# Performance work log

Hardware: AMD Instinct MI355X
Metric: run time of the kernel (lower is better)

## Reference

```python
import jax, jax.numpy as jnp
import numpy as np

SIZE = (4096, 4096)   # self.size
SIGMA = 1.0           # blur_sigma
NOISE_STD = 0.01      # noise_std


def _gauss_kernel(sigma):
    # scipy.ndimage.gaussian_filter: radius = int(truncate*sigma + 0.5), truncate=4.0
    r = int(4.0 * sigma + 0.5)
    x = np.arange(-r, r + 1, dtype=np.float32)
    k = np.exp(-0.5 * (x / sigma) ** 2)
    k = k / k.sum()
    return jnp.asarray(k), r


def _blur(img, sigma):
    # img: [C, H, W]; separable Gaussian, scipy mode='reflect' == jnp symmetric pad
    k, r = _gauss_kernel(sigma)
    x = jnp.pad(img, ((0, 0), (r, r), (r, r)), mode='symmetric')
    x = x[:, None]  # [C, 1, H+2r, W+2r] (NCHW)
    kh = k.reshape(1, 1, -1, 1)
    kw = k.reshape(1, 1, 1, -1)
    x = jax.lax.conv_general_dilated(x, kh, (1, 1), 'VALID')
    x = jax.lax.conv_general_dilated(x, kw, (1, 1), 'VALID')
    return x[:, 0]  # [C, H, W]


def setup_inputs() -> dict:
    key = jax.random.key(0)
    k1, k2 = jax.random.split(key)
    img = jax.random.normal(k1, (1, 2048, 2048), dtype=jnp.float32)
    noise = jax.random.normal(k2, (1,) + SIZE, dtype=jnp.float32)
    return {"img": img, "noise": noise}


def reference(img, noise):
    # bilinear resize, align_corners=False == jax half-pixel linear resize
    img = jax.image.resize(img, (img.shape[0],) + SIZE, method='linear')
    img = jnp.flip(img, axis=2)   # horizontal flip
    img = jnp.flip(img, axis=1)   # vertical flip
    img = jnp.rot90(img, k=1, axes=(1, 2))  # rot90, k fixed to 1
    img = img + noise * NOISE_STD
    img = _blur(img, SIGMA)
    img = jnp.log1p(jnp.clip(img, 0.0))  # clamp(min=0) then log1p
    return img
```

## Files before the change

kernel.cpp:

```cpp
#include <hip/hip_runtime.h>
#include <math.h>

#define N      4096
#define NIMG   2048
#define SPAN   128
#define TXN    120
#define HRW    16
#define PP     66
#define PR     68
#define IPOFF  (PR * PP)
#define NSX    35
#define NSY    64
#define NBLK   (NSX * NSY)

#define KW0 0.00013383063f
#define KW1 0.00443186160f
#define KW2 0.05399112800f
#define KW3 0.24197144000f
#define KW4 0.39894346870f

__device__ __forceinline__ int symi(int g) {
    g = (g < 0) ? (-1 - g) : g;
    g = (g >= N) ? (2 * N - 1 - g) : g;
    return g;
}

__device__ __forceinline__ void gload_lds4(const float* g, float* l) {
    __builtin_amdgcn_global_load_lds(
        (const __attribute__((address_space(1))) unsigned int*)g,
        (__attribute__((address_space(3))) unsigned int*)l, 4, 0, 0);
}

#define H9(A,B,C,D,E,F,G,H,I)                                                  \
    fmaf(KW0,(A), fmaf(KW1,(B), fmaf(KW2,(C), fmaf(KW3,(D), fmaf(KW4,(E),      \
    fmaf(KW3,(F), fmaf(KW2,(G), fmaf(KW1,(H), KW0*(I)))))))))

#define GCOL2(J, G) do {                                                       \
    const float p0_ = ipg[(J) - PP];                                           \
    const float p1_ = ipg[(J)];                                                \
    const float p2_ = ipg[(J) + PP];                                           \
    (G).x = fmaf(0.75f, p1_, 0.25f * p2_);                                     \
    (G).y = fmaf(0.25f, p0_, 0.75f * p1_);                                     \
} while (0)

#define PROD4(J2, D0, D1, D2, D3, Z0, Z1, Z2, Z3) do {                         \
    float2 gc_, gd_;                                                           \
    GCOL2((J2), gc_); GCOL2((J2) + 1, gd_);                                    \
    (D0).x = fmaf(0.25f, ga.x, fmaf(0.75f, gb.x, 0.01f * (Z0).x));             \
    (D0).y = fmaf(0.25f, ga.y, fmaf(0.75f, gb.y, 0.01f * (Z0).y));             \
    (D1).x = fmaf(0.75f, gb.x, fmaf(0.25f, gc_.x, 0.01f * (Z1).x));            \
    (D1).y = fmaf(0.75f, gb.y, fmaf(0.25f, gc_.y, 0.01f * (Z1).y));            \
    (D2).x = fmaf(0.25f, gb.x, fmaf(0.75f, gc_.x, 0.01f * (Z2).x));            \
    (D2).y = fmaf(0.25f, gb.y, fmaf(0.75f, gc_.y, 0.01f * (Z2).y));            \
    (D3).x = fmaf(0.75f, gc_.x, fmaf(0.25f, gd_.x, 0.01f * (Z3).x));           \
    (D3).y = fmaf(0.75f, gc_.y, fmaf(0.25f, gd_.y, 0.01f * (Z3).y));           \
    ga = gc_; gb = gd_;                                                        \
} while (0)

#define OUT1(K, GY) do {                                                       \
    float2 v_;                                                                 \
    v_.x = H9(win[K].x, win[K+1].x, win[K+2].x, win[K+3].x, win[K+4].x,        \
              win[K+5].x, win[K+6].x, win[K+7].x, win[K+8].x);                 \
    v_.y = H9(win[K].y, win[K+1].y, win[K+2].y, win[K+3].y, win[K+4].y,        \
              win[K+5].y, win[K+6].y, win[K+7].y, win[K+8].y);                 \
    float* sl_ = ((K) & 1) ? EX1 : EX0;                                        \
    *reinterpret_cast<float2*>(sl_ + 2 * lane) = v_;                           \
    const float2 l0_ = *reinterpret_cast<const float2*>(sl_ + oL0);            \
    const float2 l1_ = *reinterpret_cast<const float2*>(sl_ + oL1);            \
    const float2 r0_ = *reinterpret_cast<const float2*>(sl_ + oR0);            \
    const float2 r1_ = *reinterpret_cast<const float2*>(sl_ + oR1);            \
    float ox_ = KW0 * l0_.x; ox_ = fmaf(KW1, l0_.y, ox_);                      \
    ox_ = fmaf(KW2, l1_.x, ox_); ox_ = fmaf(KW3, l1_.y, ox_);                  \
    ox_ = fmaf(KW4, v_.x, ox_);  ox_ = fmaf(KW3, v_.y, ox_);                   \
    ox_ = fmaf(KW2, r0_.x, ox_); ox_ = fmaf(KW1, r0_.y, ox_);                  \
    ox_ = fmaf(KW0, r1_.x, ox_);                                               \
    float oy_ = KW0 * l0_.y; oy_ = fmaf(KW1, l1_.x, oy_);                      \
    oy_ = fmaf(KW2, l1_.y, oy_); oy_ = fmaf(KW3, v_.x, oy_);                   \
    oy_ = fmaf(KW4, v_.y, oy_);  oy_ = fmaf(KW3, r0_.x, oy_);                  \
    oy_ = fmaf(KW2, r0_.y, oy_); oy_ = fmaf(KW1, r1_.x, oy_);                  \
    oy_ = fmaf(KW0, r1_.y, oy_);                                               \
    float2 rr_;                                                                \
    rr_.x = __logf(1.0f + fmaxf(ox_, 0.0f));                                   \
    rr_.y = __logf(1.0f + fmaxf(oy_, 0.0f));                                   \
    if (okst) *reinterpret_cast<float2*>(out + (size_t)(GY) * N + gxs) = rr_;  \
} while (0)

#define SLIDE4() do {                                                          \
    _Pragma("unroll")                                                          \
    for (int i_ = 0; i_ < 8; ++i_) win[i_] = win[i_ + 4];                      \
} while (0)

__global__ __launch_bounds__(256, 6)
void TensorAugment_79216376807666_kernel(const float* __restrict__ img,
                                         const float* __restrict__ noise,
                                         float* __restrict__ out) {
    __shared__ __align__(16) float SH[IPOFF + 4 * 256];

    const int tid  = threadIdx.x;
    const int lane = tid & 63;
    const int wave = tid >> 6;

    float* const IP  = SH;
    float* const EX0 = SH + IPOFF + wave * 256;
    float* const EX1 = EX0 + 128;

    const int bid = blockIdx.x;
    int sx, sy;
    if (bid < 2 * NSY) { sy = bid >> 1; sx = (bid & 1) ? (NSX - 1) : 0; }
    else { const int t = bid - 2 * NSY; sx = 1 + t % (NSX - 2); sy = t / (NSX - 2); }
    const int x0 = sx * TXN;
    const int y0 = sy * 64;

    int gxa = x0 - 4, gxb = x0 + SPAN - 5;
    int mxa = symi(gxa), mxb = symi(gxb);
    int gxmin = min(mxa, mxb), gxmax = max(mxa, mxb);
    if (gxa <= 0) gxmin = 0;
    if (gxb >= N - 1) gxmax = N - 1;
    int umin = (N - 1) - gxmax, umax = (N - 1) - gxmin;
    int r0min = (umin - 1) >> 1;
    int r0max = (umax - 1) >> 1;
    int nrows = r0max - r0min + 2;

    int gya = y0 - 4, gyb = y0 + 67;
    int mya = symi(gya), myb = symi(gyb);
    int gymin = min(mya, myb), gymax = max(mya, myb);
    if (gya <= 0) gymin = 0;
    if (gyb >= N - 1) gymax = N - 1;
    int c0min = (gymin - 1) >> 1;
    (void)nrows;

    {
        const int gcol = min(max(c0min + lane, 0), NIMG - 1);
#pragma unroll
        for (int k = 0; k < 17; ++k) {
            const int r  = wave + 4 * k;
            const int ir = min(max(r0min + r, 0), NIMG - 1);
            gload_lds4(img + (size_t)ir * NIMG + gcol, IP + r * PP);
        }
    }

    const int y0w = y0 + HRW * wave;
    const int gxs = x0 - 4 + 2 * lane;
    const bool okst = (lane >= 2) && (lane <= 61) && (gxs <= N - 2);
    const bool yin  = (y0w >= 4) && (y0w + 19 <= N - 1);
    const bool xin  = (sx > 0) && (sx < NSX - 1);
    const bool fast = xin && yin;
    const int oL0 = max(2 * lane - 4, 0), oL1 = max(2 * lane - 2, 0);
    const int oR0 = min(2 * lane + 2, 126), oR1 = min(2 * lane + 4, 126);

    const int a    = (x0 >> 1) - 2 + lane;
    const int ipb  = (2047 - a - r0min) * PP;
    const float* const ipg = IP + ipb;
    const int jb   = ((y0w - 5) >> 1) - c0min;
    const float* const nzb = noise + ((size_t)(y0w - 4) * N + gxs);
#define LDNZ(DR) (*reinterpret_cast<const float2*>(nzb + (size_t)(DR) * N))

    float2 npre[12];
    if (fast) {
#pragma unroll
        for (int j = 0; j < 12; ++j) npre[j] = LDNZ(j);
    }

    __syncthreads();

    float2 win[12];

    if (fast) {
        float2 ga, gb;
        GCOL2(jb, ga);
        GCOL2(jb + 1, gb);

        PROD4(jb + 2, win[0], win[1], win[2],  win[3],  npre[0], npre[1], npre[2],  npre[3]);
        PROD4(jb + 4, win[4], win[5], win[6],  win[7],  npre[4], npre[5], npre[6],  npre[7]);
        PROD4(jb + 6, win[8], win[9], win[10], win[11], npre[8], npre[9], npre[10], npre[11]);

        {
            float2 n0 = LDNZ(12), n1 = LDNZ(13), n2 = LDNZ(14), n3 = LDNZ(15);
            OUT1(0, y0w + 0); OUT1(1, y0w + 1); OUT1(2, y0w + 2); OUT1(3, y0w + 3);
            SLIDE4();
            PROD4(jb + 8, win[8], win[9], win[10], win[11], n0, n1, n2, n3);
        }
        {
            float2 n0 = LDNZ(16), n1 = LDNZ(17), n2 = LDNZ(18), n3 = LDNZ(19);
            OUT1(0, y0w + 4); OUT1(1, y0w + 5); OUT1(2, y0w + 6); OUT1(3, y0w + 7);
            SLIDE4();
            PROD4(jb + 10, win[8], win[9], win[10], win[11], n0, n1, n2, n3);
        }
        {
            float2 n0 = LDNZ(20), n1 = LDNZ(21), n2 = LDNZ(22), n3 = LDNZ(23);
            OUT1(0, y0w + 8); OUT1(1, y0w + 9); OUT1(2, y0w + 10); OUT1(3, y0w + 11);
            SLIDE4();
            PROD4(jb + 12, win[8], win[9], win[10], win[11], n0, n1, n2, n3);
        }
        OUT1(0, y0w + 12); OUT1(1, y0w + 13); OUT1(2, y0w + 14); OUT1(3, y0w + 15);
    } else {
        const int gxm0 = symi(gxs), gxm1 = symi(gxs + 1);
        const int u0 = (N - 1) - gxm0, u1 = (N - 1) - gxm1;
        const int A0 = (((u0 - 1) >> 1) - r0min) * PP;
        const int A1 = (((u1 - 1) >> 1) - r0min) * PP;
        const float w10 = (u0 & 1) ? 0.25f : 0.75f, w00 = 1.0f - w10;
        const float w11 = (u1 & 1) ? 0.25f : 0.75f, w01 = 1.0f - w11;

        auto nzg = [&](int dr) -> float2 {
            const float* nr = noise + (size_t)symi(y0w - 4 + dr) * N;
            float2 r; r.x = nr[gxm0]; r.y = nr[gxm1]; return r;
        };
        auto dgen = [&](int dr, float2 nz) -> float2 {
            const int gym = symi(y0w - 4 + dr);
            const int jc  = ((gym - 1) >> 1) - c0min;
            const float wc1 = (gym & 1) ? 0.25f : 0.75f;
            const float wc0 = 1.0f - wc1;
            float2 r;
            {
                const float t = fmaf(wc0, IP[A0 + jc], wc1 * IP[A0 + jc + 1]);
                const float b = fmaf(wc0, IP[A0 + PP + jc], wc1 * IP[A0 + PP + jc + 1]);
                r.x = fmaf(w00, t, fmaf(w10, b, 0.01f * nz.x));
            }
            {
                const float t = fmaf(wc0, IP[A1 + jc], wc1 * IP[A1 + jc + 1]);
                const float b = fmaf(wc0, IP[A1 + PP + jc], wc1 * IP[A1 + PP + jc + 1]);
                r.y = fmaf(w01, t, fmaf(w11, b, 0.01f * nz.y));
            }
            return r;
        };

#pragma unroll
        for (int j = 0; j < 12; ++j) win[j] = dgen(j, nzg(j));

#pragma unroll
        for (int c = 0; c < 4; ++c) {
            float2 n0, n1, n2, n3;
            if (c < 3) { n0 = nzg(12 + 4 * c); n1 = nzg(13 + 4 * c);
                         n2 = nzg(14 + 4 * c); n3 = nzg(15 + 4 * c); }
            OUT1(0, y0w + 4 * c + 0); OUT1(1, y0w + 4 * c + 1);
            OUT1(2, y0w + 4 * c + 2); OUT1(3, y0w + 4 * c + 3);
            if (c < 3) {
                SLIDE4();
                win[8]  = dgen(12 + 4 * c, n0);
                win[9]  = dgen(13 + 4 * c, n1);
                win[10] = dgen(14 + 4 * c, n2);
                win[11] = dgen(15 + 4 * c, n3);
            }
        }
    }
#undef LDNZ
}

extern "C" void kernel_launch(void* const* d_in, const int* in_sizes, int n_in,
                              void* d_out, int out_size, void* d_ws, size_t ws_size,
                              hipStream_t stream) {
    const float* img   = (const float*)d_in[0];
    const float* noise = (const float*)d_in[1];
    float* out = (float*)d_out;

    dim3 grid(NBLK);
    TensorAugment_79216376807666_kernel<<<grid, 256, 0, stream>>>(img, noise, out);
}
```

Measured before the change: 144.0 us.

## Swap LDS direct loads for register staging, remap blocks per XCD, prefetch noise earlier

```diff
diff --git a/kernel.cpp b/kernel.cpp
--- a/kernel.cpp
+++ b/kernel.cpp
@@ -7,8 +7,7 @@
 #define TXN    120
 #define HRW    16
 #define PP     66
-#define PR     68
-#define IPOFF  (PR * PP)
+#define PR     66
 #define NSX    35
 #define NSY    64
 #define NBLK   (NSX * NSY)
@@ -23,12 +22,6 @@
     g = (g < 0) ? (-1 - g) : g;
     g = (g >= N) ? (2 * N - 1 - g) : g;
     return g;
-}
-
-__device__ __forceinline__ void gload_lds4(const float* g, float* l) {
-    __builtin_amdgcn_global_load_lds(
-        (const __attribute__((address_space(1))) unsigned int*)g,
-        (__attribute__((address_space(3))) unsigned int*)l, 4, 0, 0);
 }
 
 #define H9(A,B,C,D,E,F,G,H,I)                                                  \
@@ -90,26 +83,27 @@
     for (int i_ = 0; i_ < 8; ++i_) win[i_] = win[i_ + 4];                      \
 } while (0)
 
-__global__ __launch_bounds__(256, 6)
+__global__ __launch_bounds__(256, 5)
 void TensorAugment_79216376807666_kernel(const float* __restrict__ img,
                                          const float* __restrict__ noise,
                                          float* __restrict__ out) {
-    __shared__ __align__(16) float SH[IPOFF + 4 * 256];
+    __shared__ __align__(16) float SH[PR * PP + 4 * 256];
 
     const int tid  = threadIdx.x;
     const int lane = tid & 63;
     const int wave = tid >> 6;
 
     float* const IP  = SH;
-    float* const EX0 = SH + IPOFF + wave * 256;
+    float* const EX0 = SH + PR * PP + wave * 256;
     float* const EX1 = EX0 + 128;
 
-    const int bid = blockIdx.x;
-    int sx, sy;
-    if (bid < 2 * NSY) { sy = bid >> 1; sx = (bid & 1) ? (NSX - 1) : 0; }
-    else { const int t = bid - 2 * NSY; sx = 1 + t % (NSX - 2); sy = t / (NSX - 2); }
-    const int x0 = sx * TXN;
-    const int y0 = sy * 64;
+    const int bid0 = blockIdx.x;
+    const int xcd  = bid0 & 7;
+    const int ii   = bid0 >> 3;
+    const int sx   = ii % NSX;
+    const int sy   = xcd * (NSY / 8) + ii / NSX;
+    const int x0   = sx * TXN;
+    const int y0   = sy * 64;
 
     int gxa = x0 - 4, gxb = x0 + SPAN - 5;
     int mxa = symi(gxa), mxb = symi(gxb);
@@ -127,15 +121,20 @@
     if (gya <= 0) gymin = 0;
     if (gyb >= N - 1) gymax = N - 1;
     int c0min = (gymin - 1) >> 1;
-    (void)nrows;
 
     {
         const int gcol = min(max(c0min + lane, 0), NIMG - 1);
+        float sv[17];
 #pragma unroll
         for (int k = 0; k < 17; ++k) {
-            const int r  = wave + 4 * k;
+            const int r  = min(wave + 4 * k, nrows - 1);
             const int ir = min(max(r0min + r, 0), NIMG - 1);
-            gload_lds4(img + (size_t)ir * NIMG + gcol, IP + r * PP);
+            sv[k] = img[(size_t)ir * NIMG + gcol];
+        }
+#pragma unroll
+        for (int k = 0; k < 17; ++k) {
+            const int r = min(wave + 4 * k, nrows - 1);
+            IP[r * PP + lane] = sv[k];
         }
     }
 
@@ -156,9 +155,11 @@
 #define LDNZ(DR) (*reinterpret_cast<const float2*>(nzb + (size_t)(DR) * N))
 
     float2 npre[12];
+    float2 nA0, nA1, nA2, nA3;
     if (fast) {
 #pragma unroll
         for (int j = 0; j < 12; ++j) npre[j] = LDNZ(j);
+        nA0 = LDNZ(12); nA1 = LDNZ(13); nA2 = LDNZ(14); nA3 = LDNZ(15);
     }
 
     __syncthreads();
@@ -166,6 +167,8 @@
     float2 win[12];
 
     if (fast) {
+        float2 nB0 = LDNZ(16), nB1 = LDNZ(17), nB2 = LDNZ(18), nB3 = LDNZ(19);
+
         float2 ga, gb;
         GCOL2(jb, ga);
         GCOL2(jb + 1, gb);
@@ -174,24 +177,19 @@
         PROD4(jb + 4, win[4], win[5], win[6],  win[7],  npre[4], npre[5], npre[6],  npre[7]);
         PROD4(jb + 6, win[8], win[9], win[10], win[11], npre[8], npre[9], npre[10], npre[11]);
 
-        {
-            float2 n0 = LDNZ(12), n1 = LDNZ(13), n2 = LDNZ(14), n3 = LDNZ(15);
-            OUT1(0, y0w + 0); OUT1(1, y0w + 1); OUT1(2, y0w + 2); OUT1(3, y0w + 3);
-            SLIDE4();
-            PROD4(jb + 8, win[8], win[9], win[10], win[11], n0, n1, n2, n3);
-        }
-        {
-            float2 n0 = LDNZ(16), n1 = LDNZ(17), n2 = LDNZ(18), n3 = LDNZ(19);
-            OUT1(0, y0w + 4); OUT1(1, y0w + 5); OUT1(2, y0w + 6); OUT1(3, y0w + 7);
-            SLIDE4();
-            PROD4(jb + 10, win[8], win[9], win[10], win[11], n0, n1, n2, n3);
-        }
-        {
-            float2 n0 = LDNZ(20), n1 = LDNZ(21), n2 = LDNZ(22), n3 = LDNZ(23);
-            OUT1(0, y0w + 8); OUT1(1, y0w + 9); OUT1(2, y0w + 10); OUT1(3, y0w + 11);
-            SLIDE4();
-            PROD4(jb + 12, win[8], win[9], win[10], win[11], n0, n1, n2, n3);
-        }
+        float2 nC0 = LDNZ(20), nC1 = LDNZ(21), nC2 = LDNZ(22), nC3 = LDNZ(23);
+        OUT1(0, y0w + 0); OUT1(1, y0w + 1); OUT1(2, y0w + 2); OUT1(3, y0w + 3);
+        SLIDE4();
+        PROD4(jb + 8, win[8], win[9], win[10], win[11], nA0, nA1, nA2, nA3);
+
+        OUT1(0, y0w + 4); OUT1(1, y0w + 5); OUT1(2, y0w + 6); OUT1(3, y0w + 7);
+        SLIDE4();
+        PROD4(jb + 10, win[8], win[9], win[10], win[11], nB0, nB1, nB2, nB3);
+
+        OUT1(0, y0w + 8); OUT1(1, y0w + 9); OUT1(2, y0w + 10); OUT1(3, y0w + 11);
+        SLIDE4();
+        PROD4(jb + 12, win[8], win[9], win[10], win[11], nC0, nC1, nC2, nC3);
+
         OUT1(0, y0w + 12); OUT1(1, y0w + 13); OUT1(2, y0w + 14); OUT1(3, y0w + 15);
     } else {
         const int gxm0 = symi(gxs), gxm1 = symi(gxs + 1);
```

Result: faster. 138.1 us (-4.1%).
